# Performance work log

Measured on AMD Instinct MI355X. Metric: run time of the kernel, lower is better.

The kernel has to match this reference:

```python
import jax, jax.numpy as jnp
import numpy as np

D = 768           # input_dim == slot_dim
H, DH = 8, 64     # encoder attention heads / head dim (x-transformers defaults)
INNER = 4 * D     # ff_mult=4 GLU inner dim
EPS = 1e-8
N_ITERS = 3
SCALE = D ** -0.5


def _ln(x, g, b):
    m = jnp.mean(x, axis=-1, keepdims=True)
    v = jnp.var(x, axis=-1, keepdims=True)
    return (x - m) / jnp.sqrt(v + 1e-5) * g + b


def setup_inputs() -> dict:
    key = jax.random.key(0)
    ks = jax.random.split(key, 16)
    w = lambda i, shape, s=0.02: jax.random.normal(ks[i], shape, jnp.float32) * s
    return dict(
        x=jax.random.normal(ks[0], (32, 1024, D), jnp.float32),
        noise=jax.random.normal(ks[1], (32, 16, D), jnp.float32),
        init_mu=jax.random.normal(ks[2], (D,), jnp.float32),
        init_log_sigma=w(3, (D,), 0.05),
        Wk=w(4, (D, D)), Wv=w(5, (D, D)), Wq=w(6, (D, D)),
        ni_g=jnp.ones(D), ni_b=jnp.zeros(D),       # norm_input
        ns_g=jnp.ones(D), ns_b=jnp.zeros(D),       # norm_slots
        nica_g=jnp.ones(D), nica_b=jnp.zeros(D),   # norm_ica
        ln1_g=jnp.ones(D), ln1_b=jnp.zeros(D),     # encoder attn pre-norm
        Wq_a=w(7, (D, H * DH)), Wk_a=w(8, (D, H * DH)),
        Wv_a=w(9, (D, H * DH)), Wo_a=w(10, (H * DH, D)),
        ln2_g=jnp.ones(D), ln2_b=jnp.zeros(D),     # encoder ff pre-norm
        W1=w(11, (D, 2 * INNER)), W2=w(12, (INNER, D)),
        lnf_g=jnp.ones(D), lnf_b=jnp.zeros(D),     # encoder final norm
    )


def _inv_cross_attn(q, k, v):
    # softmax over the SLOT axis (dim i), then renormalize over keys j
    dots = jnp.einsum('bid,bjd->bij', q, k) * SCALE
    attn = jax.nn.softmax(dots, axis=1) + EPS
    attn = attn / jnp.sum(attn, axis=-1, keepdims=True)
    updates = jnp.einsum('bjd,bij->bid', v, attn)
    return updates, attn


def _encoder(h, ln1_g, ln1_b, Wq_a, Wk_a, Wv_a, Wo_a, ln2_g, ln2_b, W1, W2, lnf_g, lnf_b):
    b, n, _ = h.shape
    a = _ln(h, ln1_g, ln1_b)
    q = (a @ Wq_a).reshape(b, n, H, DH)
    k = (a @ Wk_a).reshape(b, n, H, DH)
    v = (a @ Wv_a).reshape(b, n, H, DH)
    scores = jnp.einsum('bihd,bjhd->bhij', q, k) * (DH ** -0.5)
    p = jax.nn.softmax(scores, axis=-1)
    o = jnp.einsum('bhij,bjhd->bihd', p, v).reshape(b, n, H * DH)
    h = h + o @ Wo_a
    f = _ln(h, ln2_g, ln2_b)
    u, g = jnp.split(f @ W1, 2, axis=-1)
    h = h + (u * jax.nn.silu(g)) @ W2
    return _ln(h, lnf_g, lnf_b)


def reference(x, noise, init_mu, init_log_sigma, Wk, Wv, Wq,
              ni_g, ni_b, ns_g, ns_b, nica_g, nica_b,
              ln1_g, ln1_b, Wq_a, Wk_a, Wv_a, Wo_a,
              ln2_g, ln2_b, W1, W2, lnf_g, lnf_b):
    xn = _ln(x, ni_g, ni_b)
    k = xn @ Wk
    v = xn @ Wv
    slots = init_mu + jnp.exp(init_log_sigma) * noise  # [b, n_slots, d]

    def step(slots):
        q = _ln(slots, ns_g, ns_b) @ Wq
        updates, attn = _inv_cross_attn(q, k, v)
        slots = _ln(slots + updates, nica_g, nica_b)
        slots = _encoder(slots, ln1_g, ln1_b, Wq_a, Wk_a, Wv_a, Wo_a,
                         ln2_g, ln2_b, W1, W2, lnf_g, lnf_b)
        return slots, attn

    for _ in range(N_ITERS):
        slots, _ = step(slots)
    slots, attn = step(slots)
    attn_map = jnp.transpose(attn, (0, 2, 1))  # b n hw -> b hw n
    return slots, attn_map
```

## Files before the change

kernel.cpp:

```cpp
#include <hip/hip_runtime.h>
#include <hip/hip_bf16.h>
#include <stdint.h>

typedef _Float16 f16;
typedef __attribute__((ext_vector_type(8))) _Float16 f16x8;
typedef __attribute__((ext_vector_type(4))) _Float16 f16x4;
typedef __attribute__((ext_vector_type(4))) float f32x4;

#define GLOBAL_AS __attribute__((address_space(1)))
#define LDS_AS __attribute__((address_space(3)))

#define D_DIM 768
#define NTOK 1024
#define NSLOT 16
#define NB 32
#define NTOT (NB*NTOK)
#define HDIM 512
#define INNER 3072
#define SCALE_D 0.03608439182435161f
#define SCALE_H 0.125f

__global__ __launch_bounds__(256) void mgemm128_k(
    const f16* __restrict__ A, const f16* __restrict__ Bt,
    f16* __restrict__ Kout, f16* __restrict__ VTout, int M, int K)
{
  __shared__ __align__(16) f16 As[128*64];
  __shared__ __align__(16) f16 Bs[128*64];
  const int tid = threadIdx.x;
  const int lane = tid & 63;
  const int wave = tid >> 6;
  const int m0 = blockIdx.y*128, n0 = blockIdx.x*128;
  const int wm = (wave>>1)*64, wn = (wave&1)*64;
  const int quad = lane>>4, l16 = lane&15;

  const int sr = tid>>2;
  const int sc = (tid&3)*8;
  const f16* gA0 = A  + (size_t)(m0 + sr)*K + sc;
  const f16* gA1 = gA0 + (size_t)64*K;
  const f16* gB0 = Bt + (size_t)(n0 + sr)*K + sc;
  const f16* gB1 = gB0 + (size_t)64*K;

  f32x4 acc[4][4] = {};

  for (int k0 = 0; k0 < K; k0 += 64){
    #pragma unroll
    for (int p=0;p<2;++p){
      __builtin_amdgcn_global_load_lds((const GLOBAL_AS void*)(gA0 + k0 + p*32),
          (LDS_AS void*)&As[p*4096 + tid*8], 16, 0, 0);
      __builtin_amdgcn_global_load_lds((const GLOBAL_AS void*)(gA1 + k0 + p*32),
          (LDS_AS void*)&As[p*4096 + (256+tid)*8], 16, 0, 0);
      __builtin_amdgcn_global_load_lds((const GLOBAL_AS void*)(gB0 + k0 + p*32),
          (LDS_AS void*)&Bs[p*4096 + tid*8], 16, 0, 0);
      __builtin_amdgcn_global_load_lds((const GLOBAL_AS void*)(gB1 + k0 + p*32),
          (LDS_AS void*)&Bs[p*4096 + (256+tid)*8], 16, 0, 0);
    }
    __syncthreads();
    #pragma unroll
    for (int p=0;p<2;++p){
      const f16* fA = &As[p*4096 + (wm + l16)*32 + quad*8];
      const f16* fB = &Bs[p*4096 + (wn + l16)*32 + quad*8];
      f16x8 a[4], b[4];
      #pragma unroll
      for (int t=0;t<4;++t) a[t] = *(const f16x8*)(fA + t*16*32);
      #pragma unroll
      for (int t=0;t<4;++t) b[t] = *(const f16x8*)(fB + t*16*32);
      #pragma unroll
      for (int mt=0;mt<4;++mt)
        #pragma unroll
        for (int nt=0;nt<4;++nt)
          acc[mt][nt] = __builtin_amdgcn_mfma_f32_16x16x32_f16(a[mt], b[nt], acc[mt][nt], 0, 0, 0);
    }
    __syncthreads();
  }

  if (n0 < 768){
    #pragma unroll
    for (int mt=0;mt<4;++mt)
      #pragma unroll
      for (int nt=0;nt<4;++nt){
        int gm = m0 + wm + mt*16 + quad*4;
        int gn = n0 + wn + nt*16 + l16;
        #pragma unroll
        for (int r=0;r<4;++r)
          Kout[(size_t)(gm+r)*768 + gn] = (f16)acc[mt][nt][r];
      }
  } else {
    #pragma unroll
    for (int mt=0;mt<4;++mt)
      #pragma unroll
      for (int nt=0;nt<4;++nt){
        int gm = m0 + wm + mt*16 + quad*4;
        int gn = n0 - 768 + wn + nt*16 + l16;
        f16x4 v4 = { (f16)acc[mt][nt][0], (f16)acc[mt][nt][1],
                     (f16)acc[mt][nt][2], (f16)acc[mt][nt][3] };
        *(f16x4*)&VTout[(size_t)gn*M + gm] = v4;
      }
  }
}

template<int OUT>
__global__ __launch_bounds__(256) void mgemm64_k(
    const f16* __restrict__ A, const f16* __restrict__ Bt,
    void* __restrict__ Cout, int M, int N, int K, int Kc)
{
  __shared__ __align__(16) f16 As[64*128];
  __shared__ __align__(16) f16 Bs[64*128];
  const int tid = threadIdx.x;
  const int lane = tid & 63;
  const int wave = tid >> 6;
  const int m0 = blockIdx.x*64, n0 = blockIdx.y*64;
  const int kbeg = blockIdx.z * Kc;
  const int wm = (wave>>1)*32, wn = (wave&1)*32;
  const int quad = lane>>4, l16 = lane&15;

  const int sr = tid>>2;
  const int sc = (tid&3)*8;
  const f16* gA = A  + (size_t)(m0+sr)*K + kbeg + sc;
  const f16* gB = Bt + (size_t)(n0+sr)*K + kbeg + sc;
  LDS_AS f16* lA = (LDS_AS f16*)&As[(size_t)tid*8];
  LDS_AS f16* lB = (LDS_AS f16*)&Bs[(size_t)tid*8];

  const f16* fA0 = &As[(wm + l16)*32 + quad*8];
  const f16* fB0 = &Bs[(wn + l16)*32 + quad*8];

  f32x4 acc[2][2] = {};

  for (int k0 = 0; k0 < Kc; k0 += 128){
    #pragma unroll
    for (int p=0;p<4;++p){
      __builtin_amdgcn_global_load_lds((const GLOBAL_AS void*)(gA + k0 + p*32),
                                       (LDS_AS void*)(lA + (size_t)p*2048), 16, 0, 0);
      __builtin_amdgcn_global_load_lds((const GLOBAL_AS void*)(gB + k0 + p*32),
                                       (LDS_AS void*)(lB + (size_t)p*2048), 16, 0, 0);
    }
    __syncthreads();
    #pragma unroll
    for (int p=0;p<4;++p){
      f16x8 a0 = *(const f16x8*)(fA0 + p*2048);
      f16x8 a1 = *(const f16x8*)(fA0 + p*2048 + 16*32);
      f16x8 b0 = *(const f16x8*)(fB0 + p*2048);
      f16x8 b1 = *(const f16x8*)(fB0 + p*2048 + 16*32);
      acc[0][0] = __builtin_amdgcn_mfma_f32_16x16x32_f16(a0,b0,acc[0][0],0,0,0);
      acc[0][1] = __builtin_amdgcn_mfma_f32_16x16x32_f16(a0,b1,acc[0][1],0,0,0);
      acc[1][0] = __builtin_amdgcn_mfma_f32_16x16x32_f16(a1,b0,acc[1][0],0,0,0);
      acc[1][1] = __builtin_amdgcn_mfma_f32_16x16x32_f16(a1,b1,acc[1][1],0,0,0);
    }
    __syncthreads();
  }
  #pragma unroll
  for (int mt=0;mt<2;++mt){
    #pragma unroll
    for (int nt=0;nt<2;++nt){
      int gm = m0 + wm + mt*16 + quad*4;
      int gn = n0 + wn + nt*16 + l16;
      #pragma unroll
      for (int r=0;r<4;++r){
        float c = acc[mt][nt][r];
        size_t idx = (size_t)(gm+r)*N + gn;
        if (OUT==0)      ((float*)Cout)[idx] = c;
        else if (OUT==1) ((f16*)Cout)[idx] = (f16)c;
        else             atomicAdd(&((float*)Cout)[idx], c);
      }
    }
  }
}

__global__ __launch_bounds__(256) void w1glu_k(
    const f16* __restrict__ A, const f16* __restrict__ W1T,
    f16* __restrict__ act, int M)
{
  __shared__ __align__(16) f16 As[64*128];
  __shared__ __align__(16) f16 Bu[64*128];
  __shared__ __align__(16) f16 Bg[64*128];
  const int K = 768;
  const int tid = threadIdx.x;
  const int lane = tid & 63;
  const int wave = tid >> 6;
  const int m0 = blockIdx.x*64, n0 = blockIdx.y*64;
  const int wm = (wave>>1)*32, wn = (wave&1)*32;
  const int quad = lane>>4, l16 = lane&15;

  const int sr = tid>>2;
  const int sc = (tid&3)*8;
  const f16* gA  = A   + (size_t)(m0+sr)*K + sc;
  const f16* gBu = W1T + (size_t)(n0+sr)*K + sc;
  const f16* gBg = W1T + (size_t)(3072+n0+sr)*K + sc;
  LDS_AS f16* lA  = (LDS_AS f16*)&As[(size_t)tid*8];
  LDS_AS f16* lBu = (LDS_AS f16*)&Bu[(size_t)tid*8];
  LDS_AS f16* lBg = (LDS_AS f16*)&Bg[(size_t)tid*8];

  const f16* fA0 = &As[(wm + l16)*32 + quad*8];
  const f16* fU0 = &Bu[(wn + l16)*32 + quad*8];
  const f16* fG0 = &Bg[(wn + l16)*32 + quad*8];

  f32x4 accU[2][2] = {};
  f32x4 accG[2][2] = {};

  for (int k0 = 0; k0 < K; k0 += 128){
    #pragma unroll
    for (int p=0;p<4;++p){
      __builtin_amdgcn_global_load_lds((const GLOBAL_AS void*)(gA  + k0 + p*32),
                                       (LDS_AS void*)(lA  + (size_t)p*2048), 16, 0, 0);
      __builtin_amdgcn_global_load_lds((const GLOBAL_AS void*)(gBu + k0 + p*32),
                                       (LDS_AS void*)(lBu + (size_t)p*2048), 16, 0, 0);
      __builtin_amdgcn_global_load_lds((const GLOBAL_AS void*)(gBg + k0 + p*32),
                                       (LDS_AS void*)(lBg + (size_t)p*2048), 16, 0, 0);
    }
    __syncthreads();
    #pragma unroll
    for (int p=0;p<4;++p){
      f16x8 a0 = *(const f16x8*)(fA0 + p*2048);
      f16x8 a1 = *(const f16x8*)(fA0 + p*2048 + 16*32);
      f16x8 u0 = *(const f16x8*)(fU0 + p*2048);
      f16x8 u1 = *(const f16x8*)(fU0 + p*2048 + 16*32);
      f16x8 g0 = *(const f16x8*)(fG0 + p*2048);
      f16x8 g1 = *(const f16x8*)(fG0 + p*2048 + 16*32);
      accU[0][0] = __builtin_amdgcn_mfma_f32_16x16x32_f16(a0,u0,accU[0][0],0,0,0);
      accU[0][1] = __builtin_amdgcn_mfma_f32_16x16x32_f16(a0,u1,accU[0][1],0,0,0);
      accU[1][0] = __builtin_amdgcn_mfma_f32_16x16x32_f16(a1,u0,accU[1][0],0,0,0);
      accU[1][1] = __builtin_amdgcn_mfma_f32_16x16x32_f16(a1,u1,accU[1][1],0,0,0);
      accG[0][0] = __builtin_amdgcn_mfma_f32_16x16x32_f16(a0,g0,accG[0][0],0,0,0);
      accG[0][1] = __builtin_amdgcn_mfma_f32_16x16x32_f16(a0,g1,accG[0][1],0,0,0);
      accG[1][0] = __builtin_amdgcn_mfma_f32_16x16x32_f16(a1,g0,accG[1][0],0,0,0);
      accG[1][1] = __builtin_amdgcn_mfma_f32_16x16x32_f16(a1,g1,accG[1][1],0,0,0);
    }
    __syncthreads();
  }
  #pragma unroll
  for (int mt=0;mt<2;++mt){
    #pragma unroll
    for (int nt=0;nt<2;++nt){
      int gm = m0 + wm + mt*16 + quad*4;
      int gn = n0 + wn + nt*16 + l16;
      #pragma unroll
      for (int r=0;r<4;++r){
        float u = accU[mt][nt][r];
        float g = accG[mt][nt][r];
        float sg = g / (1.0f + __expf(-g));
        act[(size_t)(gm+r)*INNER + gn] = (f16)(u*sg);
      }
    }
  }
}

__global__ __launch_bounds__(256) void dots_k(
    const f16* __restrict__ Q,
    const f16* __restrict__ Kh,
    f16* __restrict__ attn,
    float* __restrict__ rowsum)
{
  __shared__ __align__(16) f16 qf[16*768];
  __shared__ __align__(16) f16 ks[64*128];
  const int b = blockIdx.x, jt = blockIdx.y;
  const int tid = threadIdx.x;
  const int lane = tid & 63;
  const int w = tid >> 6;
  const int quad = lane>>4, l16 = lane&15;

  #pragma unroll
  for (int c=0;c<6;++c){
    int p = c*256 + tid;
    int ki = p >> 6, qd = (p >> 4) & 3, rw = p & 15;
    f16x8 v = *(const f16x8*)(Q + ((size_t)(b*NSLOT+rw))*D_DIM + ki*32 + qd*8);
    *(f16x8*)&qf[(size_t)p*8] = v;
  }

  const f16* gK = Kh + ((size_t)(b*NTOK + jt*64 + (tid>>2)))*D_DIM + (tid&3)*8;
  LDS_AS f16* lK = (LDS_AS f16*)&ks[(size_t)tid*8];

  f32x4 acc = {};
  for (int it=0; it<6; ++it){
    #pragma unroll
    for (int p=0;p<4;++p)
      __builtin_amdgcn_global_load_lds((const GLOBAL_AS void*)(gK + it*128 + p*32),
                                       (LDS_AS void*)(lK + (size_t)p*2048), 16, 0, 0);
    __syncthreads();
    #pragma unroll
    for (int p=0;p<4;++p){
      f16x8 a  = *(const f16x8*)&qf[(((size_t)(it*4+p)*4 + quad)*16 + l16)*8];
      f16x8 bf = *(const f16x8*)&ks[(size_t)p*2048 + (w*16+l16)*32 + quad*8];
      acc = __builtin_amdgcn_mfma_f32_16x16x32_f16(a, bf, acc, 0, 0, 0);
    }
    __syncthreads();
  }

  float v0 = acc[0]*SCALE_D, v1 = acc[1]*SCALE_D, v2 = acc[2]*SCALE_D, v3 = acc[3]*SCALE_D;
  float mx = fmaxf(fmaxf(v0,v1), fmaxf(v2,v3));
  mx = fmaxf(mx, __shfl_xor(mx, 16));
  mx = fmaxf(mx, __shfl_xor(mx, 32));
  float e0 = __expf(v0-mx), e1 = __expf(v1-mx), e2 = __expf(v2-mx), e3 = __expf(v3-mx);
  float s = e0+e1+e2+e3;
  s += __shfl_xor(s, 16);
  s += __shfl_xor(s, 32);
  float inv = 1.0f/s;
  float a0 = e0*inv + 1e-8f, a1 = e1*inv + 1e-8f, a2 = e2*inv + 1e-8f, a3 = e3*inv + 1e-8f;

  int jcol = jt*64 + w*16 + l16;
  int ibase = b*NSLOT + quad*4;
  attn[(size_t)(ibase+0)*NTOK + jcol] = (f16)a0;
  attn[(size_t)(ibase+1)*NTOK + jcol] = (f16)a1;
  attn[(size_t)(ibase+2)*NTOK + jcol] = (f16)a2;
  attn[(size_t)(ibase+3)*NTOK + jcol] = (f16)a3;

  float t0=a0, t1=a1, t2=a2, t3=a3;
  #pragma unroll
  for (int m=1;m<16;m<<=1){
    t0 += __shfl_xor(t0, m);
    t1 += __shfl_xor(t1, m);
    t2 += __shfl_xor(t2, m);
    t3 += __shfl_xor(t3, m);
  }
  if (l16 == 0){
    atomicAdd(&rowsum[ibase+0], t0);
    atomicAdd(&rowsum[ibase+1], t1);
    atomicAdd(&rowsum[ibase+2], t2);
    atomicAdd(&rowsum[ibase+3], t3);
  }
}

__global__ __launch_bounds__(256) void attnv_k(
    const f16* __restrict__ attn,
    const float* __restrict__ rowsum,
    const f16* __restrict__ VT,
    float* __restrict__ upd)
{
  __shared__ __align__(16) f16 Asl[16*128];
  __shared__ __align__(16) f16 Bsl[64*128];
  const int b = blockIdx.x, d0 = blockIdx.y*64;
  const int tid = threadIdx.x;
  const int lane = tid & 63;
  const int w = tid >> 6;
  const int quad = lane>>4, l16 = lane&15;

  const int pa = tid>>6, ta = tid&63;
  const f16* gA = attn + ((size_t)(b*NSLOT + (ta>>2)))*NTOK + pa*32 + (ta&3)*8;
  LDS_AS f16* lA = (LDS_AS f16*)&Asl[(size_t)pa*512 + ta*8];
  const f16* gB = VT + ((size_t)(d0 + (tid>>2)))*NTOT + b*NTOK + (tid&3)*8;
  LDS_AS f16* lB = (LDS_AS f16*)&Bsl[(size_t)tid*8];

  f32x4 acc = {};
  for (int it=0; it<8; ++it){
    __builtin_amdgcn_global_load_lds((const GLOBAL_AS void*)(gA + it*128),
                                     (LDS_AS void*)lA, 16, 0, 0);
    #pragma unroll
    for (int p=0;p<4;++p)
      __builtin_amdgcn_global_load_lds((const GLOBAL_AS void*)(gB + it*128 + p*32),
                                       (LDS_AS void*)(lB + (size_t)p*2048), 16, 0, 0);
    __syncthreads();
    #pragma unroll
    for (int p=0;p<4;++p){
      f16x8 a  = *(const f16x8*)&Asl[(size_t)p*512 + l16*32 + quad*8];
      f16x8 bf = *(const f16x8*)&Bsl[(size_t)p*2048 + (w*16+l16)*32 + quad*8];
      acc = __builtin_amdgcn_mfma_f32_16x16x32_f16(a, bf, acc, 0, 0, 0);
    }
    __syncthreads();
  }
  int dcol = d0 + w*16 + l16;
  #pragma unroll
  for (int r=0;r<4;++r){
    int i = b*NSLOT + quad*4 + r;
    upd[(size_t)i*D_DIM + dcol] = acc[r] / rowsum[i];
  }
}

template<bool ADD, int OUT>
__global__ __launch_bounds__(256) void ln_k(
    const float* __restrict__ X, const float* __restrict__ X2,
    const float* __restrict__ g, const float* __restrict__ bb,
    void* __restrict__ out)
{
  __shared__ float rs[256], rss[256];
  const int row = blockIdx.x, tid = threadIdx.x;
  const float* x = X + (size_t)row*D_DIM;
  float vals[3]; float s=0.f, ss=0.f;
  #pragma unroll
  for (int t=0;t<3;++t){
    int c = tid + t*256;
    float v = x[c];
    if (ADD) v += X2[(size_t)row*D_DIM + c];
    vals[t]=v; s+=v; ss+=v*v;
  }
  rs[tid]=s; rss[tid]=ss; __syncthreads();
  for (int off=128; off>0; off>>=1){
    if (tid<off){ rs[tid]+=rs[tid+off]; rss[tid]+=rss[tid+off]; }
    __syncthreads();
  }
  float mean = rs[0]*(1.0f/768.0f);
  float var  = rss[0]*(1.0f/768.0f) - mean*mean;
  float inv  = rsqrtf(var + 1e-5f);
  #pragma unroll
  for (int t=0;t<3;++t){
    int c = tid + t*256;
    float y = (vals[t]-mean)*inv*g[c] + bb[c];
    if (OUT==1) ((f16*)out)[(size_t)row*D_DIM + c] = (f16)y;
    else        ((float*)out)[(size_t)row*D_DIM + c] = y;
  }
}

template<bool ADD>
__global__ __launch_bounds__(256) void lnln_k(
    const float* __restrict__ X, const float* __restrict__ X2,
    const float* __restrict__ g1, const float* __restrict__ b1,
    const float* __restrict__ g2, const float* __restrict__ b2,
    float* __restrict__ out1, f16* __restrict__ out2)
{
  __shared__ float rs[256], rss[256];
  const int row = blockIdx.x, tid = threadIdx.x;
  const float* x = X + (size_t)row*D_DIM;
  float vals[3]; float s=0.f, ss=0.f;
  #pragma unroll
  for (int t=0;t<3;++t){
    int c = tid + t*256;
    float v = x[c];
    if (ADD) v += X2[(size_t)row*D_DIM + c];
    vals[t]=v; s+=v; ss+=v*v;
  }
  rs[tid]=s; rss[tid]=ss; __syncthreads();
  for (int off=128; off>0; off>>=1){
    if (tid<off){ rs[tid]+=rs[tid+off]; rss[tid]+=rss[tid+off]; }
    __syncthreads();
  }
  float mean = rs[0]*(1.0f/768.0f);
  float var  = rss[0]*(1.0f/768.0f) - mean*mean;
  float inv  = rsqrtf(var + 1e-5f);
  float y[3]; float s2=0.f, ss2=0.f;
  #pragma unroll
  for (int t=0;t<3;++t){
    int c = tid + t*256;
    float yy = (vals[t]-mean)*inv*g1[c] + b1[c];
    y[t]=yy; s2+=yy; ss2+=yy*yy;
    out1[(size_t)row*D_DIM + c] = yy;
  }
  __syncthreads();
  rs[tid]=s2; rss[tid]=ss2; __syncthreads();
  for (int off=128; off>0; off>>=1){
    if (tid<off){ rs[tid]+=rs[tid+off]; rss[tid]+=rss[tid+off]; }
    __syncthreads();
  }
  float mean2 = rs[0]*(1.0f/768.0f);
  float var2  = rss[0]*(1.0f/768.0f) - mean2*mean2;
  float inv2  = rsqrtf(var2 + 1e-5f);
  #pragma unroll
  for (int t=0;t<3;++t){
    int c = tid + t*256;
    out2[(size_t)row*D_DIM + c] = (f16)((y[t]-mean2)*inv2*g2[c] + b2[c]);
  }
}

__global__ __launch_bounds__(256) void slots_init_k(
    const float* __restrict__ noise, const float* __restrict__ mu,
    const float* __restrict__ ls, float* __restrict__ slots)
{
  int idx = blockIdx.x*256 + threadIdx.x;
  int d = idx % D_DIM;
  slots[idx] = mu[d] + expf(ls[d]) * noise[idx];
}

__global__ __launch_bounds__(256) void encattn_k(
    const f16* __restrict__ QA, const f16* __restrict__ KA,
    const f16* __restrict__ VA, int QSTR,
    f16* __restrict__ O)
{
  __shared__ float qs[16][68], ks[16][68], vs[16][68], ps[16][20];
  const int b = blockIdx.x, h = blockIdx.y;
  const int tid = threadIdx.x;
  {
    int i = tid>>4, dd=(tid&15)*4;
    size_t base = ((size_t)(b*NSLOT+i))*QSTR + h*64 + dd;
    f16x4 uq = *(const f16x4*)(QA + base);
    f16x4 uk = *(const f16x4*)(KA + base);
    f16x4 uv = *(const f16x4*)(VA + base);
    float4 fq = { (float)uq.x, (float)uq.y, (float)uq.z, (float)uq.w };
    float4 fk = { (float)uk.x, (float)uk.y, (float)uk.z, (float)uk.w };
    float4 fv = { (float)uv.x, (float)uv.y, (float)uv.z, (float)uv.w };
    *(float4*)&qs[i][dd]=fq; *(float4*)&ks[i][dd]=fk; *(float4*)&vs[i][dd]=fv;
  }
  __syncthreads();
  {
    int i = tid>>4, j = tid&15;
    float s=0.f;
    #pragma unroll 8
    for (int d=0; d<64; ++d) s += qs[i][d]*ks[j][d];
    ps[i][j] = s*SCALE_H;
  }
  __syncthreads();
  if (tid < 16){
    int i = tid;
    float mx=-1e30f;
    #pragma unroll
    for (int j=0;j<16;++j) mx = fmaxf(mx, ps[i][j]);
    float sm=0.f;
    #pragma unroll
    for (int j=0;j<16;++j){ float e=__expf(ps[i][j]-mx); ps[i][j]=e; sm+=e; }
    float inv=1.0f/sm;
    #pragma unroll
    for (int j=0;j<16;++j) ps[i][j]*=inv;
  }
  __syncthreads();
  {
    int i = tid>>4, dq=(tid&15)*4;
    float a0=0,a1=0,a2=0,a3=0;
    #pragma unroll
    for (int j=0;j<16;++j){
      float p = ps[i][j];
      a0+=p*vs[j][dq+0]; a1+=p*vs[j][dq+1]; a2+=p*vs[j][dq+2]; a3+=p*vs[j][dq+3];
    }
    size_t base = ((size_t)(b*NSLOT+i))*HDIM + h*64 + dq;
    O[base+0]=(f16)a0; O[base+1]=(f16)a1; O[base+2]=(f16)a2; O[base+3]=(f16)a3;
  }
}

__global__ __launch_bounds__(256) void cast_t_k(
    const float* __restrict__ in, f16* __restrict__ out, int R, int C)
{
  __shared__ float t[32][33];
  int r0 = blockIdx.x*32, c0 = blockIdx.y*32;
  int tr = threadIdx.x & 31, g8 = threadIdx.x >> 5;
  #pragma unroll
  for (int s=0;s<4;++s){
    int r = g8*4 + s;
    t[r][tr] = in[(size_t)(r0+r)*C + c0+tr];
  }
  __syncthreads();
  #pragma unroll
  for (int s=0;s<4;++s){
    int c = g8*4+s;
    out[(size_t)(c0+c)*R + r0+tr] = (f16)t[tr][c];
  }
}

__global__ __launch_bounds__(256) void attnout_k(
    const f16* __restrict__ attn, const float* __restrict__ rowsum,
    float* __restrict__ out)
{
  int idx = blockIdx.x*256 + threadIdx.x;
  int i = idx & 15;
  int j = (idx >> 4) & 1023;
  int b = idx >> 14;
  out[idx] = (float)attn[((size_t)b*NSLOT+i)*NTOK + j] / rowsum[b*NSLOT + i];
}

extern "C" void kernel_launch(void* const* d_in, const int* in_sizes, int n_in,
                              void* d_out, int out_size, void* d_ws, size_t ws_size,
                              hipStream_t stream) {
  const float* x        = (const float*)d_in[0];
  const float* noise    = (const float*)d_in[1];
  const float* init_mu  = (const float*)d_in[2];
  const float* init_ls  = (const float*)d_in[3];
  const float* Wk       = (const float*)d_in[4];
  const float* Wv       = (const float*)d_in[5];
  const float* Wq       = (const float*)d_in[6];
  const float* ni_g     = (const float*)d_in[7];
  const float* ni_b     = (const float*)d_in[8];
  const float* ns_g     = (const float*)d_in[9];
  const float* ns_b     = (const float*)d_in[10];
  const float* nica_g   = (const float*)d_in[11];
  const float* nica_b   = (const float*)d_in[12];
  const float* ln1_g    = (const float*)d_in[13];
  const float* ln1_b    = (const float*)d_in[14];
  const float* Wq_a     = (const float*)d_in[15];
  const float* Wk_a     = (const float*)d_in[16];
  const float* Wv_a     = (const float*)d_in[17];
  const float* Wo_a     = (const float*)d_in[18];
  const float* ln2_g    = (const float*)d_in[19];
  const float* ln2_b    = (const float*)d_in[20];
  const float* W1       = (const float*)d_in[21];
  const float* W2       = (const float*)d_in[22];
  const float* lnf_g    = (const float*)d_in[23];
  const float* lnf_b    = (const float*)d_in[24];

  char* w = (char*)d_ws;
  size_t off = 0;
  auto alloc = [&](size_t bytes)->char*{
    char* p = w + off; off += (bytes + 255) & ~(size_t)255; return p;
  };
  f16* xn_h  = (f16*)alloc((size_t)NTOT*D_DIM*2);
  f16* k_h   = (f16*)alloc((size_t)NTOT*D_DIM*2);
  f16* vT_h  = (f16*)alloc((size_t)D_DIM*NTOT*2);
  f16* WkvT  = (f16*)alloc((size_t)1536*768*2);
  f16* WqT   = (f16*)alloc((size_t)768*768*2);
  f16* WqkvT = (f16*)alloc((size_t)1536*768*2);
  f16* WoaT  = (f16*)alloc((size_t)768*512*2);
  f16* W1T   = (f16*)alloc((size_t)6144*768*2);
  f16* W2T   = (f16*)alloc((size_t)768*3072*2);
  float* slots = (float*)alloc(512*768*4);
  float* hbuf  = (float*)alloc(512*768*4);
  float* upd   = (float*)alloc(512*768*4);
  f16* tmp_h  = (f16*)alloc(512*768*2);
  f16* tmp2_h = (f16*)alloc(512*768*2);
  f16* q_h    = (f16*)alloc(512*768*2);
  f16* qkv_h  = (f16*)alloc((size_t)512*1536*2);
  f16* o_h    = (f16*)alloc(512*512*2);
  f16* act_h  = (f16*)alloc((size_t)512*3072*2);
  f16* attn_h = (f16*)alloc((size_t)NB*NSLOT*NTOK*2);
  float* rowsum = (float*)alloc(512*4);

  auto castT = [&](const float* src, f16* dst, int R, int C){
    cast_t_k<<<dim3(R/32, C/32), 256, 0, stream>>>(src, dst, R, C);
  };
  castT(Wk,   WkvT,            768, 768);
  castT(Wv,   WkvT + 768*768,  768, 768);
  castT(Wq,   WqT,             768, 768);
  castT(Wq_a, WqkvT,             768, 512);
  castT(Wk_a, WqkvT + 512*768,   768, 512);
  castT(Wv_a, WqkvT + 1024*768,  768, 512);
  castT(Wo_a, WoaT,            512, 768);
  castT(W1,   W1T,             768, 6144);
  castT(W2,   W2T,             3072, 768);

  ln_k<false,1><<<NTOT, 256, 0, stream>>>(x, nullptr, ni_g, ni_b, xn_h);
  mgemm128_k<<<dim3(1536/128, NTOT/128), 256, 0, stream>>>(xn_h, WkvT, k_h, vT_h, NTOT, 768);

  slots_init_k<<<512*768/256, 256, 0, stream>>>(noise, init_mu, init_ls, slots);
  ln_k<false,1><<<512, 256, 0, stream>>>(slots, nullptr, ns_g, ns_b, tmp2_h);

  for (int it=0; it<4; ++it){
    hipMemsetAsync(rowsum, 0, 512*4, stream);
    mgemm64_k<1><<<dim3(8, 12, 1), 256, 0, stream>>>(tmp2_h, WqT, q_h, 512, 768, 768, 768);
    dots_k<<<dim3(NB, 16), 256, 0, stream>>>(q_h, k_h, attn_h, rowsum);
    attnv_k<<<dim3(NB, 12), 256, 0, stream>>>(attn_h, rowsum, vT_h, upd);
    lnln_k<true><<<512, 256, 0, stream>>>(slots, upd, nica_g, nica_b, ln1_g, ln1_b, hbuf, tmp_h);
    mgemm64_k<1><<<dim3(8, 24, 1), 256, 0, stream>>>(tmp_h, WqkvT, qkv_h, 512, 1536, 768, 768);
    encattn_k<<<dim3(NB, 8), 256, 0, stream>>>(qkv_h, qkv_h + 512, qkv_h + 1024, 1536, o_h);
    mgemm64_k<2><<<dim3(8, 12, 2), 256, 0, stream>>>(o_h, WoaT, hbuf, 512, 768, 512, 256);
    ln_k<false,1><<<512, 256, 0, stream>>>(hbuf, nullptr, ln2_g, ln2_b, tmp_h);
    w1glu_k<<<dim3(8, 48), 256, 0, stream>>>(tmp_h, W1T, act_h, 512);
    mgemm64_k<2><<<dim3(8, 12, 4), 256, 0, stream>>>(act_h, W2T, hbuf, 512, 768, 3072, 768);
    lnln_k<false><<<512, 256, 0, stream>>>(hbuf, nullptr, lnf_g, lnf_b, ns_g, ns_b, slots, tmp2_h);
  }

  hipMemcpyAsync(d_out, slots, (size_t)512*768*4, hipMemcpyDeviceToDevice, stream);
  attnout_k<<<NB*NTOK*NSLOT/256, 256, 0, stream>>>(attn_h, rowsum, (float*)d_out + 512*768);
}
```

Measured before the change: 742.3 us.

## Fold Wk into query projection and apply Wv after attention to skip K/V GEMMs

Rather than projecting all 32K tokens through Wk and Wv, the code precomputes Wq·Wkᵀ so queries attend directly to normalized inputs, and applies Wv to the small attention-weighted sum afterward. This removes the large token-level K/V GEMM in favor of a transpose of xn plus an extra small GEMM per iteration. Row sums now go to per-tile partial buffers reduced in-kernel instead of global atomics with a memset. The risk is a different fp16 rounding path through the fused weight product.

```diff
diff --git a/kernel.cpp b/kernel.cpp
--- a/kernel.cpp
+++ b/kernel.cpp
@@ -19,84 +19,6 @@
 #define INNER 3072
 #define SCALE_D 0.03608439182435161f
 #define SCALE_H 0.125f
-
-__global__ __launch_bounds__(256) void mgemm128_k(
-    const f16* __restrict__ A, const f16* __restrict__ Bt,
-    f16* __restrict__ Kout, f16* __restrict__ VTout, int M, int K)
-{
-  __shared__ __align__(16) f16 As[128*64];
-  __shared__ __align__(16) f16 Bs[128*64];
-  const int tid = threadIdx.x;
-  const int lane = tid & 63;
-  const int wave = tid >> 6;
-  const int m0 = blockIdx.y*128, n0 = blockIdx.x*128;
-  const int wm = (wave>>1)*64, wn = (wave&1)*64;
-  const int quad = lane>>4, l16 = lane&15;
-
-  const int sr = tid>>2;
-  const int sc = (tid&3)*8;
-  const f16* gA0 = A  + (size_t)(m0 + sr)*K + sc;
-  const f16* gA1 = gA0 + (size_t)64*K;
-  const f16* gB0 = Bt + (size_t)(n0 + sr)*K + sc;
-  const f16* gB1 = gB0 + (size_t)64*K;
-
-  f32x4 acc[4][4] = {};
-
-  for (int k0 = 0; k0 < K; k0 += 64){
-    #pragma unroll
-    for (int p=0;p<2;++p){
-      __builtin_amdgcn_global_load_lds((const GLOBAL_AS void*)(gA0 + k0 + p*32),
-          (LDS_AS void*)&As[p*4096 + tid*8], 16, 0, 0);
-      __builtin_amdgcn_global_load_lds((const GLOBAL_AS void*)(gA1 + k0 + p*32),
-          (LDS_AS void*)&As[p*4096 + (256+tid)*8], 16, 0, 0);
-      __builtin_amdgcn_global_load_lds((const GLOBAL_AS void*)(gB0 + k0 + p*32),
-          (LDS_AS void*)&Bs[p*4096 + tid*8], 16, 0, 0);
-      __builtin_amdgcn_global_load_lds((const GLOBAL_AS void*)(gB1 + k0 + p*32),
-          (LDS_AS void*)&Bs[p*4096 + (256+tid)*8], 16, 0, 0);
-    }
-    __syncthreads();
-    #pragma unroll
-    for (int p=0;p<2;++p){
-      const f16* fA = &As[p*4096 + (wm + l16)*32 + quad*8];
-      const f16* fB = &Bs[p*4096 + (wn + l16)*32 + quad*8];
-      f16x8 a[4], b[4];
-      #pragma unroll
-      for (int t=0;t<4;++t) a[t] = *(const f16x8*)(fA + t*16*32);
-      #pragma unroll
-      for (int t=0;t<4;++t) b[t] = *(const f16x8*)(fB + t*16*32);
-      #pragma unroll
-      for (int mt=0;mt<4;++mt)
-        #pragma unroll
-        for (int nt=0;nt<4;++nt)
-          acc[mt][nt] = __builtin_amdgcn_mfma_f32_16x16x32_f16(a[mt], b[nt], acc[mt][nt], 0, 0, 0);
-    }
-    __syncthreads();
-  }
-
-  if (n0 < 768){
-    #pragma unroll
-    for (int mt=0;mt<4;++mt)
-      #pragma unroll
-      for (int nt=0;nt<4;++nt){
-        int gm = m0 + wm + mt*16 + quad*4;
-        int gn = n0 + wn + nt*16 + l16;
-        #pragma unroll
-        for (int r=0;r<4;++r)
-          Kout[(size_t)(gm+r)*768 + gn] = (f16)acc[mt][nt][r];
-      }
-  } else {
-    #pragma unroll
-    for (int mt=0;mt<4;++mt)
-      #pragma unroll
-      for (int nt=0;nt<4;++nt){
-        int gm = m0 + wm + mt*16 + quad*4;
-        int gn = n0 - 768 + wn + nt*16 + l16;
-        f16x4 v4 = { (f16)acc[mt][nt][0], (f16)acc[mt][nt][1],
-                     (f16)acc[mt][nt][2], (f16)acc[mt][nt][3] };
-        *(f16x4*)&VTout[(size_t)gn*M + gm] = v4;
-      }
-  }
-}
 
 template<int OUT>
 __global__ __launch_bounds__(256) void mgemm64_k(
@@ -245,12 +167,13 @@
 
 __global__ __launch_bounds__(256) void dots_k(
     const f16* __restrict__ Q,
-    const f16* __restrict__ Kh,
+    const f16* __restrict__ Xn,
     f16* __restrict__ attn,
-    float* __restrict__ rowsum)
+    float* __restrict__ rsPart)
 {
   __shared__ __align__(16) f16 qf[16*768];
   __shared__ __align__(16) f16 ks[64*128];
+  __shared__ float rpart[4][16];
   const int b = blockIdx.x, jt = blockIdx.y;
   const int tid = threadIdx.x;
   const int lane = tid & 63;
@@ -265,7 +188,7 @@
     *(f16x8*)&qf[(size_t)p*8] = v;
   }
 
-  const f16* gK = Kh + ((size_t)(b*NTOK + jt*64 + (tid>>2)))*D_DIM + (tid&3)*8;
+  const f16* gK = Xn + ((size_t)(b*NTOK + jt*64 + (tid>>2)))*D_DIM + (tid&3)*8;
   LDS_AS f16* lK = (LDS_AS f16*)&ks[(size_t)tid*8];
 
   f32x4 acc = {};
@@ -311,31 +234,44 @@
     t3 += __shfl_xor(t3, m);
   }
   if (l16 == 0){
-    atomicAdd(&rowsum[ibase+0], t0);
-    atomicAdd(&rowsum[ibase+1], t1);
-    atomicAdd(&rowsum[ibase+2], t2);
-    atomicAdd(&rowsum[ibase+3], t3);
+    rpart[w][quad*4+0] = t0;
+    rpart[w][quad*4+1] = t1;
+    rpart[w][quad*4+2] = t2;
+    rpart[w][quad*4+3] = t3;
+  }
+  __syncthreads();
+  if (tid < 16){
+    float ss = rpart[0][tid] + rpart[1][tid] + rpart[2][tid] + rpart[3][tid];
+    rsPart[(size_t)((b*16 + jt)<<4) + tid] = ss;
   }
 }
 
 __global__ __launch_bounds__(256) void attnv_k(
     const f16* __restrict__ attn,
-    const float* __restrict__ rowsum,
-    const f16* __restrict__ VT,
-    float* __restrict__ upd)
+    const float* __restrict__ rsPart,
+    const f16* __restrict__ XnT,
+    f16* __restrict__ t_out)
 {
   __shared__ __align__(16) f16 Asl[16*128];
   __shared__ __align__(16) f16 Bsl[64*128];
+  __shared__ float rsum[16];
   const int b = blockIdx.x, d0 = blockIdx.y*64;
   const int tid = threadIdx.x;
   const int lane = tid & 63;
   const int w = tid >> 6;
   const int quad = lane>>4, l16 = lane&15;
 
+  if (tid < 16){
+    float s = 0.f;
+    #pragma unroll
+    for (int jt=0;jt<16;++jt) s += rsPart[(size_t)((b*16 + jt)<<4) + tid];
+    rsum[tid] = s;
+  }
+
   const int pa = tid>>6, ta = tid&63;
   const f16* gA = attn + ((size_t)(b*NSLOT + (ta>>2)))*NTOK + pa*32 + (ta&3)*8;
   LDS_AS f16* lA = (LDS_AS f16*)&Asl[(size_t)pa*512 + ta*8];
-  const f16* gB = VT + ((size_t)(d0 + (tid>>2)))*NTOT + b*NTOK + (tid&3)*8;
+  const f16* gB = XnT + ((size_t)(d0 + (tid>>2)))*NTOT + b*NTOK + (tid&3)*8;
   LDS_AS f16* lB = (LDS_AS f16*)&Bsl[(size_t)tid*8];
 
   f32x4 acc = {};
@@ -358,8 +294,8 @@
   int dcol = d0 + w*16 + l16;
   #pragma unroll
   for (int r=0;r<4;++r){
-    int i = b*NSLOT + quad*4 + r;
-    upd[(size_t)i*D_DIM + dcol] = acc[r] / rowsum[i];
+    int i = quad*4 + r;
+    t_out[(size_t)(b*NSLOT + i)*D_DIM + dcol] = (f16)(acc[r] / rsum[i]);
   }
 }
 
@@ -526,6 +462,50 @@
   for (int s=0;s<4;++s){
     int c = g8*4+s;
     out[(size_t)(c0+c)*R + r0+tr] = (f16)t[tr][c];
+  }
+}
+
+__global__ __launch_bounds__(256) void cast_k(
+    const float* __restrict__ in, f16* __restrict__ out, int n)
+{
+  int i = blockIdx.x*256 + threadIdx.x;
+  if (i < n) out[i] = (f16)in[i];
+}
+
+__global__ __launch_bounds__(256) void transp_k(
+    const f16* __restrict__ in, f16* __restrict__ out, int R, int C)
+{
+  __shared__ f16 T[64][72];
+  const int m0 = blockIdx.x*64, d0 = blockIdx.y*64;
+  const int tid = threadIdx.x;
+  {
+    int r = tid>>2, c = (tid&3)*16;
+    const f16* p = in + (size_t)(m0+r)*C + d0 + c;
+    *(f16x8*)&T[r][c]   = *(const f16x8*)p;
+    *(f16x8*)&T[r][c+8] = *(const f16x8*)(p+8);
+  }
+  __syncthreads();
+  {
+    int dd = tid>>2, mq = (tid&3)*16;
+    f16 v[16];
+    #pragma unroll
+    for (int e=0;e<16;++e) v[e] = T[mq+e][dd];
+    f16* p = out + (size_t)(d0+dd)*R + m0 + mq;
+    *(f16x8*)p     = *(f16x8*)&v[0];
+    *(f16x8*)(p+8) = *(f16x8*)&v[8];
+  }
+}
+
+__global__ __launch_bounds__(256) void rsfin_k(
+    const float* __restrict__ rsPart, float* __restrict__ rowsum)
+{
+  int idx = blockIdx.x*256 + threadIdx.x;
+  if (idx < 512){
+    int b = idx>>4, i = idx&15;
+    float s = 0.f;
+    #pragma unroll
+    for (int jt=0;jt<16;++jt) s += rsPart[(size_t)((b*16+jt)<<4) + i];
+    rowsum[idx] = s;
   }
 }
 
@@ -575,10 +555,11 @@
     char* p = w + off; off += (bytes + 255) & ~(size_t)255; return p;
   };
   f16* xn_h  = (f16*)alloc((size_t)NTOT*D_DIM*2);
-  f16* k_h   = (f16*)alloc((size_t)NTOT*D_DIM*2);
-  f16* vT_h  = (f16*)alloc((size_t)D_DIM*NTOT*2);
-  f16* WkvT  = (f16*)alloc((size_t)1536*768*2);
-  f16* WqT   = (f16*)alloc((size_t)768*768*2);
+  f16* xnT_h = (f16*)alloc((size_t)D_DIM*NTOT*2);
+  f16* Wkf   = (f16*)alloc((size_t)768*768*2);
+  f16* Wqf   = (f16*)alloc((size_t)768*768*2);
+  f16* BtQK  = (f16*)alloc((size_t)768*768*2);
+  f16* WvT   = (f16*)alloc((size_t)768*768*2);
   f16* WqkvT = (f16*)alloc((size_t)1536*768*2);
   f16* WoaT  = (f16*)alloc((size_t)768*512*2);
   f16* W1T   = (f16*)alloc((size_t)6144*768*2);
@@ -589,18 +570,20 @@
   f16* tmp_h  = (f16*)alloc(512*768*2);
   f16* tmp2_h = (f16*)alloc(512*768*2);
   f16* q_h    = (f16*)alloc(512*768*2);
+  f16* t_h    = (f16*)alloc(512*768*2);
   f16* qkv_h  = (f16*)alloc((size_t)512*1536*2);
   f16* o_h    = (f16*)alloc(512*512*2);
   f16* act_h  = (f16*)alloc((size_t)512*3072*2);
   f16* attn_h = (f16*)alloc((size_t)NB*NSLOT*NTOK*2);
+  float* rsPart = (float*)alloc((size_t)32*16*16*4);
   float* rowsum = (float*)alloc(512*4);
 
   auto castT = [&](const float* src, f16* dst, int R, int C){
     cast_t_k<<<dim3(R/32, C/32), 256, 0, stream>>>(src, dst, R, C);
   };
-  castT(Wk,   WkvT,            768, 768);
-  castT(Wv,   WkvT + 768*768,  768, 768);
-  castT(Wq,   WqT,             768, 768);
+  cast_k<<<768*768/256, 256, 0, stream>>>(Wk, Wkf, 768*768);
+  cast_k<<<768*768/256, 256, 0, stream>>>(Wq, Wqf, 768*768);
+  castT(Wv,   WvT,             768, 768);
   castT(Wq_a, WqkvT,             768, 512);
   castT(Wk_a, WqkvT + 512*768,   768, 512);
   castT(Wv_a, WqkvT + 1024*768,  768, 512);
@@ -608,17 +591,19 @@
   castT(W1,   W1T,             768, 6144);
   castT(W2,   W2T,             3072, 768);
 
+  mgemm64_k<1><<<dim3(12, 12, 1), 256, 0, stream>>>(Wkf, Wqf, BtQK, 768, 768, 768, 768);
+
   ln_k<false,1><<<NTOT, 256, 0, stream>>>(x, nullptr, ni_g, ni_b, xn_h);
-  mgemm128_k<<<dim3(1536/128, NTOT/128), 256, 0, stream>>>(xn_h, WkvT, k_h, vT_h, NTOT, 768);
+  transp_k<<<dim3(NTOT/64, D_DIM/64), 256, 0, stream>>>(xn_h, xnT_h, NTOT, D_DIM);
 
   slots_init_k<<<512*768/256, 256, 0, stream>>>(noise, init_mu, init_ls, slots);
   ln_k<false,1><<<512, 256, 0, stream>>>(slots, nullptr, ns_g, ns_b, tmp2_h);
 
   for (int it=0; it<4; ++it){
-    hipMemsetAsync(rowsum, 0, 512*4, stream);
-    mgemm64_k<1><<<dim3(8, 12, 1), 256, 0, stream>>>(tmp2_h, WqT, q_h, 512, 768, 768, 768);
-    dots_k<<<dim3(NB, 16), 256, 0, stream>>>(q_h, k_h, attn_h, rowsum);
-    attnv_k<<<dim3(NB, 12), 256, 0, stream>>>(attn_h, rowsum, vT_h, upd);
+    mgemm64_k<1><<<dim3(8, 12, 1), 256, 0, stream>>>(tmp2_h, BtQK, q_h, 512, 768, 768, 768);
+    dots_k<<<dim3(NB, 16), 256, 0, stream>>>(q_h, xn_h, attn_h, rsPart);
+    attnv_k<<<dim3(NB, 12), 256, 0, stream>>>(attn_h, rsPart, xnT_h, t_h);
+    mgemm64_k<0><<<dim3(8, 12, 1), 256, 0, stream>>>(t_h, WvT, upd, 512, 768, 768, 768);
     lnln_k<true><<<512, 256, 0, stream>>>(slots, upd, nica_g, nica_b, ln1_g, ln1_b, hbuf, tmp_h);
     mgemm64_k<1><<<dim3(8, 24, 1), 256, 0, stream>>>(tmp_h, WqkvT, qkv_h, 512, 1536, 768, 768);
     encattn_k<<<dim3(NB, 8), 256, 0, stream>>>(qkv_h, qkv_h + 512, qkv_h + 1024, 1536, o_h);
@@ -630,5 +615,6 @@
   }
 
   hipMemcpyAsync(d_out, slots, (size_t)512*768*4, hipMemcpyDeviceToDevice, stream);
+  rsfin_k<<<2, 256, 0, stream>>>(rsPart, rowsum);
   attnout_k<<<NB*NTOK*NSLOT/256, 256, 0, stream>>>(attn_h, rowsum, (float*)d_out + 512*768);
 }
```

After: 668.3 us. 10.0% less time.
